# Optimization experiments

Measured on AMD Instinct MI355X. Metric: run time of the kernel, lower is better.

## Reference

```python
import jax, jax.numpy as jnp
import numpy as np

OBSERVE = 30

def setup_inputs() -> dict:
    key = jax.random.key(0)
    k1, k2, k3, k4 = jax.random.split(key, 4)
    B, T = 8192, 2048
    u = jax.random.normal(k1, (B, T, 1), dtype=jnp.float32)
    x0 = jax.random.normal(k2, (B, OBSERVE), dtype=jnp.float32)
    # scale weights small so the linear AR recurrence stays stable over T steps
    W_x = jax.random.normal(k3, (OBSERVE, 1), dtype=jnp.float32) * 0.05
    W_f = jax.random.normal(k4, (1, 1), dtype=jnp.float32)
    return {"u": u, "x0": x0, "W_x": W_x, "W_f": W_f}


def reference(u, x0, W_x, W_f):
    # u: [B, T, 1]; x0: [B, observe] initial shift-register state.
    # Per step (matching the Keras cell):
    #   out = x_set @ W_x + u_t @ W_f            -> [B, 1]
    #   x_set <- concat(x_set[:, 1:], out)        (shift register)
    def step(x_set, u_t):
        out = x_set @ W_x + u_t @ W_f            # [B, 1]
        x_new = jnp.concatenate([x_set[:, 1:], out], axis=1)
        return x_new, out

    u_tbf = jnp.swapaxes(u, 0, 1)                # [T, B, 1]
    _, outs = jax.lax.scan(step, x0, u_tbf)      # outs: [T, B, 1]
    return jnp.swapaxes(outs, 0, 1)              # [B, T, 1]
```

## Files before the change

### kernel.cpp

```cpp
#include <hip/hip_runtime.h>

#define NB   8192
#define NT   2048
#define OBS  30
#define CCH  32
#define RPB  8
#define NTHR 256
#define CSTR 68

typedef float v2f __attribute__((ext_vector_type(2)));

__device__ __forceinline__ v2f step2(float (&r)[32], const v2f (&wxp)[OBS],
                                     float w29, int j, float uw0, float uw1) {
  v2f a0 = {uw0, uw1};
  v2f a1 = {0.f, 0.f};
  v2f a2 = {0.f, 0.f};
  #pragma unroll
  for (int m = 0; m < OBS; m += 3) {
    float r0 = r[(j + m) & 31], r1 = r[(j + m + 1) & 31], r2 = r[(j + m + 2) & 31];
    a0 = __builtin_elementwise_fma(wxp[m],     (v2f){r0, r0}, a0);
    a1 = __builtin_elementwise_fma(wxp[m + 1], (v2f){r1, r1}, a1);
    a2 = __builtin_elementwise_fma(wxp[m + 2], (v2f){r2, r2}, a2);
  }
  v2f A = (a0 + a1) + a2;
  float o0 = A.x;
  float o1 = fmaf(w29, o0, A.y);
  r[(j + 30) & 31] = o0;
  r[(j + 31) & 31] = o1;
  return (v2f){o0, o1};
}

__device__ __forceinline__ float dot15(const v2f (&cp)[15], const v2f (&sv)[16],
                                       float p) {
  v2f a0 = cp[0] * sv[0];
  v2f a1 = cp[1] * sv[1];
  v2f a2 = cp[2] * sv[2];
  #pragma unroll
  for (int m = 3; m < 15; m += 3) {
    a0 = __builtin_elementwise_fma(cp[m],     sv[m],     a0);
    a1 = __builtin_elementwise_fma(cp[m + 1], sv[m + 1], a1);
    a2 = __builtin_elementwise_fma(cp[m + 2], sv[m + 2], a2);
  }
  v2f A = (a0 + a1) + a2;
  return (A.x + A.y) + p;
}

__global__ void __launch_bounds__(NTHR, 2)
k_fused(const float* __restrict__ u, const float* __restrict__ x0,
        const float* __restrict__ Wx, const float* __restrict__ Wf,
        float* __restrict__ out) {
  __shared__ float tile[RPB * CCH * CSTR];
  __shared__ float Cb[64 * 33];
  __shared__ float sbuf[RPB * 32];
  const int tid  = threadIdx.x;
  const int wv   = tid >> 6;
  const int lane = tid & 63;
  const int half = lane >> 5;
  const int k    = lane & 31;
  const int row0 = blockIdx.x * RPB;
  const int lr   = wv * 2 + half;
  const int row  = row0 + lr;

  v2f wxp[OBS];
  wxp[0] = (v2f){Wx[0], 0.f};
  #pragma unroll
  for (int m = 1; m < OBS; ++m) wxp[m] = (v2f){Wx[m], Wx[m - 1]};
  const float w29 = wxp[29].x;
  const float wf  = Wf[0];

  float4 stg[16];
  const float* ub = u + ((size_t)row0 + 2 * wv) * NT;
  #pragma unroll
  for (int i = 0; i < 16; ++i) {
    int v = i * 64 + lane, rr = v >> 9, p = v & 511;
    stg[i] = *(const float4*)(ub + (size_t)rr * NT + 4 * p);
  }

  {
    float r[32];
    #pragma unroll
    for (int i = 0; i < 32; ++i) r[i] = (k < OBS && i == k) ? 1.f : 0.f;
    #pragma unroll
    for (int s = 0; s < 32; ++s) {
      v2f o = step2(r, wxp, w29, (2 * s) & 31, 0.f, 0.f);
      if (tid < OBS) {
        Cb[(2 * s) * 33 + tid]     = o.x;
        Cb[(2 * s + 1) * 33 + tid] = o.y;
      }
    }
  }
  sbuf[lr * 32 + k] = (k < OBS) ? x0[(size_t)row * OBS + k] : 0.f;

  float* sub = &tile[(wv * 2 * CCH) * CSTR];
  #pragma unroll
  for (int i = 0; i < 16; ++i) {
    int v = i * 64 + lane, rr = v >> 9, p = v & 511;
    int c = p >> 4, q = p & 15;
    *(float4*)(&sub[(rr * CCH + c) * CSTR + 4 * q]) = stg[i];
  }
  __syncthreads();

  v2f c0p[15], c1p[15];
  #pragma unroll
  for (int m = 0; m < 15; ++m)
    c0p[m] = (v2f){Cb[(2 * k) * 33 + 2 * m], Cb[(2 * k) * 33 + 2 * m + 1]};
  #pragma unroll
  for (int m = 0; m < 15; ++m)
    c1p[m] = (v2f){Cb[(2 * k + 1) * 33 + 2 * m], Cb[(2 * k + 1) * 33 + 2 * m + 1]};

  {
    float r[32];
    #pragma unroll
    for (int i = 0; i < 32; ++i) r[i] = 0.f;
    float* tc = &sub[lane * CSTR];
    #pragma unroll
    for (int q = 0; q < 16; ++q) {
      float4 u4 = *(const float4*)(tc + 4 * q);
      v2f oA = step2(r, wxp, w29, (4 * q)     & 31, wf * u4.x, wf * u4.y);
      v2f oB = step2(r, wxp, w29, (4 * q + 2) & 31, wf * u4.z, wf * u4.w);
      *(float4*)(tc + 4 * q) = make_float4(oA.x, oA.y, oB.x, oB.y);
    }
  }
  __builtin_amdgcn_wave_barrier();

  float* sl = &sbuf[lr * 32];
  const float* trow = &sub[half * CCH * CSTR];
  float* orow = out + (size_t)row * NT;
  float2 pq = *(const float2*)(&trow[2 * k]);
  #pragma unroll 1
  for (int c = 0; c < CCH; ++c) {
    v2f sv2[16];
    #pragma unroll
    for (int q = 0; q < 8; ++q) {
      float4 v = *(const float4*)(sl + 4 * q);
      sv2[2 * q]     = (v2f){v.x, v.y};
      sv2[2 * q + 1] = (v2f){v.z, v.w};
    }
    float2 pqn = pq;
    if (c + 1 < CCH)
      pqn = *(const float2*)(&trow[(c + 1) * CSTR + 2 * k]);
    float t0 = dot15(c0p, sv2, pq.x);
    float t1 = dot15(c1p, sv2, pq.y);
    if (k >= 17)
      *(float2*)(&sl[2 * k - 34]) = make_float2(t0, t1);
    *(float2*)(&orow[c * 64 + 2 * k]) = make_float2(t0, t1);
    pq = pqn;
    __builtin_amdgcn_wave_barrier();
  }
}

extern "C" void kernel_launch(void* const* d_in, const int* in_sizes, int n_in,
                              void* d_out, int out_size, void* d_ws, size_t ws_size,
                              hipStream_t stream) {
  const float* u  = (const float*)d_in[0];
  const float* x0 = (const float*)d_in[1];
  const float* Wx = (const float*)d_in[2];
  const float* Wf = (const float*)d_in[3];
  float* out = (float*)d_out;

  hipLaunchKernelGGL(k_fused, dim3(NB / RPB), dim3(NTHR), 0, stream,
                     u, x0, Wx, Wf, out);
}
```

Measured before the change: 46.38 us.

## Shrink blocks to a single wave and drop block-wide barriers

Each block now handles two rows with a single 64-thread wave instead of eight rows with four waves. All __syncthreads calls are replaced by wave barriers. The C-matrix scratch buffer is reused from the tile region, and its coefficients are read into registers before u is staged in. This removes cross-wave synchronization and shrinks LDS per block, which allows more resident blocks. The cost is four times as many blocks, each redundantly computing the 64x30 C matrix.

After: 49.70 us. +7.2%, slower.

```diff
diff --git a/kernel.cpp b/kernel.cpp
--- a/kernel.cpp
+++ b/kernel.cpp
@@ -4,8 +4,6 @@
 #define NT   2048
 #define OBS  30
 #define CCH  32
-#define RPB  8
-#define NTHR 256
 #define CSTR 68
 
 typedef float v2f __attribute__((ext_vector_type(2)));
@@ -45,21 +43,17 @@
   return (A.x + A.y) + p;
 }
 
-__global__ void __launch_bounds__(NTHR, 2)
+__global__ void __launch_bounds__(64, 2)
 k_fused(const float* __restrict__ u, const float* __restrict__ x0,
         const float* __restrict__ Wx, const float* __restrict__ Wf,
         float* __restrict__ out) {
-  __shared__ float tile[RPB * CCH * CSTR];
-  __shared__ float Cb[64 * 33];
-  __shared__ float sbuf[RPB * 32];
-  const int tid  = threadIdx.x;
-  const int wv   = tid >> 6;
-  const int lane = tid & 63;
+  __shared__ float tile[2 * CCH * CSTR];
+  __shared__ float sbuf[2 * 32];
+  const int lane = threadIdx.x;
   const int half = lane >> 5;
   const int k    = lane & 31;
-  const int row0 = blockIdx.x * RPB;
-  const int lr   = wv * 2 + half;
-  const int row  = row0 + lr;
+  const int row0 = blockIdx.x * 2;
+  const int row  = row0 + half;
 
   v2f wxp[OBS];
   wxp[0] = (v2f){Wx[0], 0.f};
@@ -69,7 +63,7 @@
   const float wf  = Wf[0];
 
   float4 stg[16];
-  const float* ub = u + ((size_t)row0 + 2 * wv) * NT;
+  const float* ub = u + (size_t)row0 * NT;
   #pragma unroll
   for (int i = 0; i < 16; ++i) {
     int v = i * 64 + lane, rr = v >> 9, p = v & 511;
@@ -83,36 +77,38 @@
     #pragma unroll
     for (int s = 0; s < 32; ++s) {
       v2f o = step2(r, wxp, w29, (2 * s) & 31, 0.f, 0.f);
-      if (tid < OBS) {
-        Cb[(2 * s) * 33 + tid]     = o.x;
-        Cb[(2 * s + 1) * 33 + tid] = o.y;
+      if (lane < OBS) {
+        tile[(2 * s) * 33 + lane]     = o.x;
+        tile[(2 * s + 1) * 33 + lane] = o.y;
       }
     }
   }
-  sbuf[lr * 32 + k] = (k < OBS) ? x0[(size_t)row * OBS + k] : 0.f;
+  __builtin_amdgcn_wave_barrier();
 
-  float* sub = &tile[(wv * 2 * CCH) * CSTR];
+  v2f c0p[15], c1p[15];
+  #pragma unroll
+  for (int m = 0; m < 15; ++m)
+    c0p[m] = (v2f){tile[(2 * k) * 33 + 2 * m], tile[(2 * k) * 33 + 2 * m + 1]};
+  #pragma unroll
+  for (int m = 0; m < 15; ++m)
+    c1p[m] = (v2f){tile[(2 * k + 1) * 33 + 2 * m],
+                   tile[(2 * k + 1) * 33 + 2 * m + 1]};
+  sbuf[half * 32 + k] = (k < OBS) ? x0[(size_t)row * OBS + k] : 0.f;
+  __builtin_amdgcn_wave_barrier();
+
   #pragma unroll
   for (int i = 0; i < 16; ++i) {
     int v = i * 64 + lane, rr = v >> 9, p = v & 511;
     int c = p >> 4, q = p & 15;
-    *(float4*)(&sub[(rr * CCH + c) * CSTR + 4 * q]) = stg[i];
+    *(float4*)(&tile[(rr * CCH + c) * CSTR + 4 * q]) = stg[i];
   }
-  __syncthreads();
-
-  v2f c0p[15], c1p[15];
-  #pragma unroll
-  for (int m = 0; m < 15; ++m)
-    c0p[m] = (v2f){Cb[(2 * k) * 33 + 2 * m], Cb[(2 * k) * 33 + 2 * m + 1]};
-  #pragma unroll
-  for (int m = 0; m < 15; ++m)
-    c1p[m] = (v2f){Cb[(2 * k + 1) * 33 + 2 * m], Cb[(2 * k + 1) * 33 + 2 * m + 1]};
+  __builtin_amdgcn_wave_barrier();
 
   {
     float r[32];
     #pragma unroll
     for (int i = 0; i < 32; ++i) r[i] = 0.f;
-    float* tc = &sub[lane * CSTR];
+    float* tc = &tile[lane * CSTR];
     #pragma unroll
     for (int q = 0; q < 16; ++q) {
       float4 u4 = *(const float4*)(tc + 4 * q);
@@ -123,8 +119,8 @@
   }
   __builtin_amdgcn_wave_barrier();
 
-  float* sl = &sbuf[lr * 32];
-  const float* trow = &sub[half * CCH * CSTR];
+  float* sl = &sbuf[half * 32];
+  const float* trow = &tile[half * CCH * CSTR];
   float* orow = out + (size_t)row * NT;
   float2 pq = *(const float2*)(&trow[2 * k]);
   #pragma unroll 1
@@ -158,6 +154,6 @@
   const float* Wf = (const float*)d_in[3];
   float* out = (float*)d_out;
 
-  hipLaunchKernelGGL(k_fused, dim3(NB / RPB), dim3(NTHR), 0, stream,
+  hipLaunchKernelGGL(k_fused, dim3(NB / 2), dim3(64), 0, stream,
                      u, x0, Wx, Wf, out);
 }
```
